# Performance work log

Hardware: AMD Instinct MI355X
Metric: run time of the kernel (lower is better)

The kernel has to match this reference:

```python
import jax, jax.numpy as jnp
import numpy as np

PI = float(np.pi)

def setup_inputs() -> dict:
    key = jax.random.key(0)
    k1, k2 = jax.random.split(key)
    inp = jax.random.normal(k1, (16, 4096, 512), dtype=jnp.float32)
    lengths = jax.random.randint(k2, (16,), 0, 4096, dtype=jnp.int32)
    return {"inp": inp, "lengths": lengths}

def reference(inp, lengths):
    B, S, D = inp.shape
    pos = jnp.arange(S, dtype=jnp.float32)                      # [S]
    lens = lengths.astype(jnp.float32)[:, None]                  # [B,1]
    safe_len = jnp.maximum(lens, 1.0)
    # cos(x / len * pi) for x < len, else 0 (matches torch.zeros init)
    pe = jnp.where(pos[None, :] < lens,
                   jnp.cos(pos[None, :] / safe_len * PI),
                   0.0)                                          # [B,S]
    pe = pe.astype(inp.dtype)
    # original intent: concatenate positional channel along feature dim
    return jnp.concatenate([inp, pe[:, :, None]], axis=2)        # [B,S,D+1]
```

## Files before the change

### kernel.cpp

```cpp
#include <hip/hip_runtime.h>
#include <hip/hip_bf16.h>
#include <math.h>


#define PB 16
#define PS 4096
#define PD 512
#define ROWS_PER_BLOCK 8
#define IN_DW   (ROWS_PER_BLOCK * PD)
#define OUT_DW  (ROWS_PER_BLOCK * (PD + 1))
#define IN_F4   (IN_DW / 4)
#define OUT_F4  (OUT_DW / 4)
#define NBLOCKS ((PB * PS) / ROWS_PER_BLOCK)
#define PI_F 3.14159265358979323846f

__global__ __launch_bounds__(256) void sinpe_kernel(
    const float4* __restrict__ in4,
    const int* __restrict__ lengths,
    float4* __restrict__ out4)
{
    __shared__ __align__(16) float lds[OUT_DW];

    const int blk = blockIdx.x;
    const int t   = threadIdx.x;

    const float4* __restrict__ in_base = in4 + (size_t)blk * IN_F4;
    #pragma unroll
    for (int j = 0; j < 4; ++j) {
        const int f = j * 256 + t;
        const float4 v = in_base[f];
        const int D = f * 4;
        const int r = D >> 9;
        const int c = D & (PD - 1);
        float* p = &lds[r * (PD + 1) + c];
        p[0] = v.x; p[1] = v.y; p[2] = v.z; p[3] = v.w;
    }

    if (t < ROWS_PER_BLOCK) {
        const int row = blk * ROWS_PER_BLOCK + t;
        const int s   = row & (PS - 1);
        const int b   = row >> 12;
        const int len = lengths[b];
        float pe = 0.0f;
        if (s < len) {
            pe = cosf(((float)s / fmaxf((float)len, 1.0f)) * PI_F);
        }
        lds[t * (PD + 1) + PD] = pe;
    }

    __syncthreads();

    float4* __restrict__ out_base = out4 + (size_t)blk * OUT_F4;
    const float4* __restrict__ lds4 = (const float4*)lds;
    #pragma unroll
    for (int j = 0; j < 5; ++j) {
        const int o = j * 256 + t;
        if (o < OUT_F4) {
            out_base[o] = lds4[o];
        }
    }
}

extern "C" void kernel_launch(void* const* d_in, const int* in_sizes, int n_in,
                              void* d_out, int out_size, void* d_ws, size_t ws_size,
                              hipStream_t stream)
{
    const float4* in4     = (const float4*)d_in[0];
    const int*    lengths = (const int*)d_in[1];
    float4*       out4    = (float4*)d_out;

    sinpe_kernel<<<NBLOCKS, 256, 0, stream>>>(in4, lengths, out4);
}
```

Before: 231.6 us.

## Drop LDS staging; gather misaligned output float4s directly from global input

Removes the shared-memory staging buffer and barrier. Each thread now computes its output float4 directly by loading two adjacent input float4s and selecting lanes by offset, splicing in the cosine positional value at row ends. Rows per block rise from 8 to 16. The aim is to cut the LDS round trip and the sync, at the cost of reading each input float4 about twice (mostly absorbed by cache), a per-element divide-by-513 and select logic.

Result: slower. 238.9 us (+3.2%).

```diff
diff --git a/kernel.cpp b/kernel.cpp
--- a/kernel.cpp
+++ b/kernel.cpp
@@ -6,12 +6,11 @@
 #define PB 16
 #define PS 4096
 #define PD 512
-#define ROWS_PER_BLOCK 8
-#define IN_DW   (ROWS_PER_BLOCK * PD)
-#define OUT_DW  (ROWS_PER_BLOCK * (PD + 1))
-#define IN_F4   (IN_DW / 4)
-#define OUT_F4  (OUT_DW / 4)
-#define NBLOCKS ((PB * PS) / ROWS_PER_BLOCK)
+#define RPB 16
+#define OUT_F4_BLK (RPB * (PD + 1) / 4)
+#define IN_F4_BLK  (RPB * PD / 4)
+#define NBLOCKS ((PB * PS) / RPB)
+#define MAX_IN_F4 (PB * PS * PD / 4)
 #define PI_F 3.14159265358979323846f
 
 __global__ __launch_bounds__(256) void sinpe_kernel(
@@ -19,44 +18,52 @@
     const int* __restrict__ lengths,
     float4* __restrict__ out4)
 {
-    __shared__ __align__(16) float lds[OUT_DW];
-
     const int blk = blockIdx.x;
     const int t   = threadIdx.x;
 
-    const float4* __restrict__ in_base = in4 + (size_t)blk * IN_F4;
+    const float4* __restrict__ inb  = in4  + (size_t)blk * IN_F4_BLK;
+    float4* __restrict__       outb = out4 + (size_t)blk * OUT_F4_BLK;
+    const int last_in = (MAX_IN_F4 - 1) - blk * IN_F4_BLK;
+
     #pragma unroll
-    for (int j = 0; j < 4; ++j) {
-        const int f = j * 256 + t;
-        const float4 v = in_base[f];
-        const int D = f * 4;
-        const int r = D >> 9;
-        const int c = D & (PD - 1);
-        float* p = &lds[r * (PD + 1) + c];
-        p[0] = v.x; p[1] = v.y; p[2] = v.z; p[3] = v.w;
-    }
+    for (int j = 0; j < 9; ++j) {
+        const int o = j * 256 + t;
+        if (o < OUT_F4_BLK) {
+            const unsigned q = 4u * (unsigned)o;
+            const unsigned r = q / 513u;
+            const unsigned c = q - 513u * r;
+            const int wd  = (int)(q - r);
+            const int ia  = wd >> 2;
+            int ib = ia + 1; if (ib > last_in) ib = last_in;
+            const float4 A = inb[ia];
+            const float4 B = inb[ib];
+            const int off = wd & 3;
 
-    if (t < ROWS_PER_BLOCK) {
-        const int row = blk * ROWS_PER_BLOCK + t;
-        const int s   = row & (PS - 1);
-        const int b   = row >> 12;
-        const int len = lengths[b];
-        float pe = 0.0f;
-        if (s < len) {
-            pe = cosf(((float)s / fmaxf((float)len, 1.0f)) * PI_F);
-        }
-        lds[t * (PD + 1) + PD] = pe;
-    }
+            const bool o1 = (off == 1), o2 = (off == 2), o3 = (off == 3);
+            float s0 = o1 ? A.y : (o2 ? A.z : (o3 ? A.w : A.x));
+            float s1 = o1 ? A.z : (o2 ? A.w : (o3 ? B.x : A.y));
+            float s2 = o1 ? A.w : (o2 ? B.x : (o3 ? B.y : A.z));
+            float s3 = o1 ? B.x : (o2 ? B.y : (o3 ? B.z : A.w));
 
-    __syncthreads();
-
-    float4* __restrict__ out_base = out4 + (size_t)blk * OUT_F4;
-    const float4* __restrict__ lds4 = (const float4*)lds;
-    #pragma unroll
-    for (int j = 0; j < 5; ++j) {
-        const int o = j * 256 + t;
-        if (o < OUT_F4) {
-            out_base[o] = lds4[o];
+            float4 v;
+            if (c <= 508u) {
+                v.x = s0; v.y = s1; v.z = s2; v.w = s3;
+            } else {
+                const int kpe  = 512 - (int)c;
+                const int rowg = blk * RPB + (int)r;
+                const int s    = rowg & (PS - 1);
+                const int b    = rowg >> 12;
+                const int len  = lengths[b];
+                float pe = 0.0f;
+                if (s < len) {
+                    pe = cosf(((float)s / fmaxf((float)len, 1.0f)) * PI_F);
+                }
+                v.x = (kpe == 0) ? pe : s0;
+                v.y = (kpe == 1) ? pe : ((kpe == 0) ? s0 : s1);
+                v.z = (kpe == 2) ? pe : ((kpe == 3) ? s2 : s1);
+                v.w = (kpe == 3) ? pe : s2;
+            }
+            outb[o] = v;
         }
     }
 }
```
